# Optimization experiments

Measured on AMD Instinct MI355X. Metric: run time of the kernel, lower is better.

Reference implementation:

```python
import jax, jax.numpy as jnp
import numpy as np

EPS = 1e-15        # norm / denominator clamp (matches geoopt min_norm)
BALL_EPS = 1e-5    # projection margin: max radius = (1-BALL_EPS)/sqrt(c)
TANH_ARG_MAX = 15.0  # pre-expmap tangent clip so tanh arg stays finite
ATANH_MAX = 1.0 - 1e-7

def _norm(x):
    return jnp.maximum(jnp.linalg.norm(x, axis=-1, keepdims=True), EPS)

def pre_clip(x, c):
    # clip tangent norm so sqrt(c)*||x|| <= TANH_ARG_MAX before expmap0
    maxn = TANH_ARG_MAX / jnp.sqrt(c)
    n = _norm(x)
    return x * jnp.minimum(1.0, maxn / n)

def post_clip(x, c):
    # project onto the open Poincare ball of curvature c
    maxn = (1.0 - BALL_EPS) / jnp.sqrt(c)
    n = _norm(x)
    return x * jnp.minimum(1.0, maxn / n)

def expmap0(u, c):
    sc = jnp.sqrt(c)
    n = _norm(u)
    return jnp.tanh(sc * n) * u / (sc * n)

def logmap0(y, c):
    sc = jnp.sqrt(c)
    n = _norm(y)
    return jnp.arctanh(jnp.minimum(sc * n, ATANH_MAX)) * y / (sc * n)

def mobius_add(x, y, c):
    x2 = jnp.sum(x * x, axis=-1, keepdims=True)
    y2 = jnp.sum(y * y, axis=-1, keepdims=True)
    xy = jnp.sum(x * y, axis=-1, keepdims=True)
    num = (1.0 + 2.0 * c * xy + c * y2) * x + (1.0 - c * x2) * y
    den = 1.0 + 2.0 * c * xy + (c * c) * x2 * y2
    return num / jnp.maximum(den, EPS)

def mobius_scalar_mul(r, x, c):
    sc = jnp.sqrt(c)
    n = _norm(x)
    return jnp.tanh(r * jnp.arctanh(jnp.minimum(sc * n, ATANH_MAX))) * x / (sc * n)


def setup_inputs() -> dict:
    key = jax.random.key(0)
    kx, ky = jax.random.split(key)
    B, N, D = 64, 577, 768
    # scale so points land well inside the ball after expmap0
    x = jax.random.normal(kx, (B, N, D), dtype=jnp.float32) * 0.05
    y = jax.random.normal(ky, (B, N, D), dtype=jnp.float32) * 0.05
    return {
        "x": x,
        "y": y,
        "curv_hra": jnp.asarray(np.log(np.e - 1.0), dtype=jnp.float32),  # inv_softplus(1.0)
        "gamma_raw": jnp.asarray(0.5, dtype=jnp.float32),
        "gamma_scale": jnp.asarray(0.0, dtype=jnp.float32),
        "scale_center": jnp.asarray(0.0, dtype=jnp.float32),
    }


def reference(x, y, curv_hra, gamma_raw, gamma_scale, scale_center):
    c = jax.nn.softplus(curv_hra)  # ball curvature from raw param
    hr_x = post_clip(expmap0(pre_clip(x, c), c), c)
    hr_y = post_clip(expmap0(pre_clip(y, c), c), c)
    s = jax.nn.sigmoid(scale_center)
    g_max = 1.0 + jax.nn.softplus(gamma_scale)
    gamma = g_max * jnp.tanh(gamma_raw)
    # learned Mobius midpoint p between hr_x and hr_y
    sx = post_clip(mobius_scalar_mul(s, hr_x, c), c)
    sy = post_clip(mobius_scalar_mul(1.0 - s, hr_y, c), c)
    p = post_clip(mobius_add(sx, sy, c), c)
    # recenter at p, scale residual branch, add, move back, log to tangent
    x_p = post_clip(mobius_add(-p, hr_x, c), c)
    y_p = post_clip(mobius_add(-p, hr_y, c), c)
    y_s = post_clip(mobius_scalar_mul(gamma, y_p, c), c)
    hres_p = post_clip(mobius_add(x_p, y_s, c), c)
    hres = mobius_add(p, hres_p, c)
    r = post_clip(hres, c)
    return logmap0(r, c)
```

## Files before the change

kernel.cpp:

```cpp
#include <hip/hip_runtime.h>
#include <math.h>

#define F_EPS 1e-15f
#define F_BALL 0.99999f
#define F_TANH_ARG_MAX 15.0f
#define F_ATANH_MAX (1.0f - 1e-7f)
#define F_LOG2E 1.4426950408889634f
#define F_LN2   0.6931471805599453f

__device__ __forceinline__ float rcp_fast(float x) {
    float r = __builtin_amdgcn_rcpf(x);
    return r * (2.0f - x * r);
}
__device__ __forceinline__ float sqrt_fast(float x) { return __builtin_amdgcn_sqrtf(x); }
__device__ __forceinline__ float exp2_fast(float x) { return __builtin_amdgcn_exp2f(x); }
__device__ __forceinline__ float log2_fast(float x) { return __builtin_amdgcn_logf(x); }
__device__ __forceinline__ float exp_fast(float x)  { return exp2_fast(x * F_LOG2E); }

__device__ __forceinline__ float tanh_fast(float x) {
    float ax = fabsf(x);
    float t  = exp2_fast(ax * (-2.0f * F_LOG2E));
    float r  = (1.0f - t) * rcp_fast(1.0f + t);
    return copysignf(r, x);
}
__device__ __forceinline__ float atanh_fast(float z) {
    return (0.5f * F_LN2) * log2_fast((1.0f + z) * rcp_fast(1.0f - z));
}
__device__ __forceinline__ float softplus_fast(float x) {
    return F_LN2 * log2_fast(1.0f + exp2_fast(x * F_LOG2E));
}

struct GramS { float X2, Y2, XY; };

__device__ __forceinline__ float gnorm2(const GramS& g, float a, float b) {
    return fmaxf(a * a * g.X2 + 2.0f * a * b * g.XY + b * b * g.Y2, 0.0f);
}
__device__ __forceinline__ float gdot(const GramS& g, float au, float bu, float av, float bv) {
    return au * av * g.X2 + (au * bv + bu * av) * g.XY + bu * bv * g.Y2;
}

__device__ __forceinline__ void madd_c(float c, float u2, float v2, float uv,
                                       float au, float bu, float av, float bv,
                                       float& ao, float& bo) {
    float twocuv = 2.0f * c * uv;
    float A = 1.0f + twocuv + c * v2;
    float B = 1.0f - c * u2;
    float rden = rcp_fast(fmaxf(1.0f + twocuv + c * c * u2 * v2, F_EPS));
    ao = (A * au + B * av) * rden;
    bo = (A * bu + B * bv) * rden;
}

__device__ __forceinline__ float pclip(const GramS& g, float maxn_post, float& a, float& b) {
    float n = fmaxf(sqrt_fast(gnorm2(g, a, b)), F_EPS);
    float s = fminf(1.0f, maxn_post * rcp_fast(n));
    a *= s; b *= s;
    return s * n;
}

__device__ __forceinline__ float msm_coef(float sc, float rcp_sc, float r,
                                          float n_in, float& n_out) {
    float ne = fmaxf(n_in, F_EPS);
    float z  = fminf(sc * ne, F_ATANH_MAX);
    float w  = tanh_fast(r * atanh_fast(z));
    float m  = w * rcp_fast(sc * ne);
    float aw = fabsf(w);
    float s  = fminf(1.0f, F_BALL * rcp_fast(fmaxf(aw, F_EPS)));
    n_out = s * aw * rcp_sc;
    return m * s;
}

__device__ __forceinline__ float hr_c(float nx, float sc, float rcp_sc,
                                      float maxn_pre, float& n_out) {
    float s1 = fminf(1.0f, maxn_pre * rcp_fast(nx));
    float n1 = fmaxf(s1 * nx, F_EPS);
    float t  = tanh_fast(sc * n1);
    float f1 = t * rcp_fast(sc * n1);
    float s2 = fminf(1.0f, F_BALL * rcp_fast(fmaxf(t, F_EPS)));
    n_out = s2 * t * rcp_sc;
    return s1 * f1 * s2;
}

__global__ __launch_bounds__(256) void hra_kernel(
    const float* __restrict__ x, const float* __restrict__ y,
    const float* __restrict__ p_curv, const float* __restrict__ p_graw,
    const float* __restrict__ p_gscale, const float* __restrict__ p_scent,
    float* __restrict__ out, int rows)
{
    const int wid  = (blockIdx.x << 2) | (threadIdx.x >> 6);
    const int lane = threadIdx.x & 63;
    const int row0 = wid << 2;
    if (row0 >= rows) return;

    const float curv   = p_curv[0];
    const float graw   = p_graw[0];
    const float gscale = p_gscale[0];
    const float scent  = p_scent[0];

    int ridx[4];
#pragma unroll
    for (int r = 0; r < 4; ++r) ridx[r] = min(row0 + r, rows - 1);

    float4 xv[4][3], yv[4][3];
#pragma unroll
    for (int r = 0; r < 4; ++r) {
        const float4* xr = (const float4*)(x + (size_t)ridx[r] * 768);
        const float4* yr = (const float4*)(y + (size_t)ridx[r] * 768);
#pragma unroll
        for (int j = 0; j < 3; ++j) {
            xv[r][j] = xr[lane + 64 * j];
            yv[r][j] = yr[lane + 64 * j];
        }
    }

    float X2[4], Y2[4], XY[4];
#pragma unroll
    for (int r = 0; r < 4; ++r) {
        float sxx = 0.0f, syy = 0.0f, sxy = 0.0f;
#pragma unroll
        for (int j = 0; j < 3; ++j) {
            sxx += xv[r][j].x * xv[r][j].x + xv[r][j].y * xv[r][j].y
                 + xv[r][j].z * xv[r][j].z + xv[r][j].w * xv[r][j].w;
            syy += yv[r][j].x * yv[r][j].x + yv[r][j].y * yv[r][j].y
                 + yv[r][j].z * yv[r][j].z + yv[r][j].w * yv[r][j].w;
            sxy += xv[r][j].x * yv[r][j].x + xv[r][j].y * yv[r][j].y
                 + xv[r][j].z * yv[r][j].z + xv[r][j].w * yv[r][j].w;
        }
        X2[r] = sxx; Y2[r] = syy; XY[r] = sxy;
    }

#pragma unroll
    for (int o = 32; o > 0; o >>= 1) {
#pragma unroll
        for (int r = 0; r < 4; ++r) {
            X2[r] += __shfl_xor(X2[r], o, 64);
            Y2[r] += __shfl_xor(Y2[r], o, 64);
            XY[r] += __shfl_xor(XY[r], o, 64);
        }
    }

    const int rsel = lane & 3;
    const float gX2 = rsel == 0 ? X2[0] : rsel == 1 ? X2[1] : rsel == 2 ? X2[2] : X2[3];
    const float gY2 = rsel == 0 ? Y2[0] : rsel == 1 ? Y2[1] : rsel == 2 ? Y2[2] : Y2[3];
    const float gXY = rsel == 0 ? XY[0] : rsel == 1 ? XY[1] : rsel == 2 ? XY[2] : XY[3];
    GramS g; g.X2 = gX2; g.Y2 = gY2; g.XY = gXY;

    const float c      = softplus_fast(curv);
    const float sc     = sqrt_fast(c);
    const float rcp_sc = rcp_fast(sc);
    const float maxn_pre  = F_TANH_ARG_MAX * rcp_sc;
    const float maxn_post = F_BALL * rcp_sc;
    const float s      = rcp_fast(1.0f + exp_fast(-scent));
    const float g_max  = 1.0f + softplus_fast(gscale);
    const float gamma  = g_max * tanh_fast(graw);

    const float nx = fmaxf(sqrt_fast(gX2), F_EPS);
    const float ny = fmaxf(sqrt_fast(gY2), F_EPS);

    float n_hx, n_hy;
    const float hx = hr_c(nx, sc, rcp_sc, maxn_pre, n_hx);
    const float hy = hr_c(ny, sc, rcp_sc, maxn_pre, n_hy);

    float n_sx, n_sy;
    const float sxa = hx * msm_coef(sc, rcp_sc, s,        n_hx, n_sx);
    const float syb = hy * msm_coef(sc, rcp_sc, 1.0f - s, n_hy, n_sy);

    float pa, pb;
    {
        float u2 = n_sx * n_sx, v2 = n_sy * n_sy;
        float uv = sxa * syb * gXY;
        madd_c(c, u2, v2, uv, sxa, 0.0f, 0.0f, syb, pa, pb);
    }
    const float n_p = pclip(g, maxn_post, pa, pb);
    const float np2 = n_p * n_p;

    float xpa, xpb;
    {
        float v2 = n_hx * n_hx;
        float uv = -hx * (pa * gX2 + pb * gXY);
        madd_c(c, np2, v2, uv, -pa, -pb, hx, 0.0f, xpa, xpb);
    }
    const float n_xp = pclip(g, maxn_post, xpa, xpb);

    float ypa, ypb;
    {
        float v2 = n_hy * n_hy;
        float uv = -hy * (pa * gXY + pb * gY2);
        madd_c(c, np2, v2, uv, -pa, -pb, 0.0f, hy, ypa, ypb);
    }
    float n_yp = pclip(g, maxn_post, ypa, ypb);

    float n_ys;
    {
        float m = msm_coef(sc, rcp_sc, gamma, n_yp, n_ys);
        ypa *= m; ypb *= m;
    }

    float ha, hb;
    {
        float u2 = n_xp * n_xp, v2 = n_ys * n_ys;
        float uv = gdot(g, xpa, xpb, ypa, ypb);
        madd_c(c, u2, v2, uv, xpa, xpb, ypa, ypb, ha, hb);
    }
    const float n_h = pclip(g, maxn_post, ha, hb);

    float ra, rb;
    {
        float u2 = np2, v2 = n_h * n_h;
        float uv = gdot(g, pa, pb, ha, hb);
        madd_c(c, u2, v2, uv, pa, pb, ha, hb, ra, rb);
    }
    const float n_r = pclip(g, maxn_post, ra, rb);

    const float nrr = fmaxf(n_r, F_EPS);
    const float z   = fminf(sc * nrr, F_ATANH_MAX);
    const float f   = atanh_fast(z) * rcp_fast(sc * nrr);
    const float fa  = f * ra;
    const float fb  = f * rb;

#pragma unroll
    for (int r = 0; r < 4; ++r) {
        const float far = __shfl(fa, r, 64);
        const float fbr = __shfl(fb, r, 64);
        if (row0 + r < rows) {
            float4* outr = (float4*)(out + (size_t)(row0 + r) * 768);
#pragma unroll
            for (int j = 0; j < 3; ++j) {
                float4 o;
                o.x = far * xv[r][j].x + fbr * yv[r][j].x;
                o.y = far * xv[r][j].y + fbr * yv[r][j].y;
                o.z = far * xv[r][j].z + fbr * yv[r][j].z;
                o.w = far * xv[r][j].w + fbr * yv[r][j].w;
                outr[lane + 64 * j] = o;
            }
        }
    }
}

extern "C" void kernel_launch(void* const* d_in, const int* in_sizes, int n_in,
                              void* d_out, int out_size, void* d_ws, size_t ws_size,
                              hipStream_t stream) {
    const float* x = (const float*)d_in[0];
    const float* y = (const float*)d_in[1];
    const float* curv = (const float*)d_in[2];
    const float* graw = (const float*)d_in[3];
    const float* gscale = (const float*)d_in[4];
    const float* scent = (const float*)d_in[5];
    float* out = (float*)d_out;

    const int rows = in_sizes[0] / 768;
    const int blocks = (rows + 15) / 16;

    hipLaunchKernelGGL(hra_kernel, dim3(blocks), dim3(256), 0, stream,
                       x, y, curv, graw, gscale, scent, out, rows);
}
```

Before: 280.2 us.

## Split fused kernel into per-row coefficient pass and streaming blend pass

Adds a first kernel that computes per-row Gram sums and the scalar coefficients (fa, fb) into the workspace, and a second grid-stride kernel that reads x and y again and writes fa*x + fb*y. The aim is to decouple the latency-heavy scalar chain from the streaming output write. The cost is that x and y are read from memory twice instead of once, and there is an extra launch. The original fused kernel remains as a fallback when no workspace is available.

```diff
diff --git a/kernel.cpp b/kernel.cpp
--- a/kernel.cpp
+++ b/kernel.cpp
@@ -80,6 +80,179 @@
     return s1 * f1 * s2;
 }
 
+__device__ __forceinline__ void chain_4rows(
+    float gX2, float gY2, float gXY,
+    float curv, float graw, float gscale, float scent,
+    float& fa, float& fb)
+{
+    GramS g; g.X2 = gX2; g.Y2 = gY2; g.XY = gXY;
+
+    const float c      = softplus_fast(curv);
+    const float sc     = sqrt_fast(c);
+    const float rcp_sc = rcp_fast(sc);
+    const float maxn_pre  = F_TANH_ARG_MAX * rcp_sc;
+    const float maxn_post = F_BALL * rcp_sc;
+    const float s      = rcp_fast(1.0f + exp_fast(-scent));
+    const float g_max  = 1.0f + softplus_fast(gscale);
+    const float gamma  = g_max * tanh_fast(graw);
+
+    const float nx = fmaxf(sqrt_fast(gX2), F_EPS);
+    const float ny = fmaxf(sqrt_fast(gY2), F_EPS);
+
+    float n_hx, n_hy;
+    const float hx = hr_c(nx, sc, rcp_sc, maxn_pre, n_hx);
+    const float hy = hr_c(ny, sc, rcp_sc, maxn_pre, n_hy);
+
+    float n_sx, n_sy;
+    const float sxa = hx * msm_coef(sc, rcp_sc, s,        n_hx, n_sx);
+    const float syb = hy * msm_coef(sc, rcp_sc, 1.0f - s, n_hy, n_sy);
+
+    float pa, pb;
+    {
+        float u2 = n_sx * n_sx, v2 = n_sy * n_sy;
+        float uv = sxa * syb * gXY;
+        madd_c(c, u2, v2, uv, sxa, 0.0f, 0.0f, syb, pa, pb);
+    }
+    const float n_p = pclip(g, maxn_post, pa, pb);
+    const float np2 = n_p * n_p;
+
+    float xpa, xpb;
+    {
+        float v2 = n_hx * n_hx;
+        float uv = -hx * (pa * gX2 + pb * gXY);
+        madd_c(c, np2, v2, uv, -pa, -pb, hx, 0.0f, xpa, xpb);
+    }
+    const float n_xp = pclip(g, maxn_post, xpa, xpb);
+
+    float ypa, ypb;
+    {
+        float v2 = n_hy * n_hy;
+        float uv = -hy * (pa * gXY + pb * gY2);
+        madd_c(c, np2, v2, uv, -pa, -pb, 0.0f, hy, ypa, ypb);
+    }
+    float n_yp = pclip(g, maxn_post, ypa, ypb);
+
+    float n_ys;
+    {
+        float m = msm_coef(sc, rcp_sc, gamma, n_yp, n_ys);
+        ypa *= m; ypb *= m;
+    }
+
+    float ha, hb;
+    {
+        float u2 = n_xp * n_xp, v2 = n_ys * n_ys;
+        float uv = gdot(g, xpa, xpb, ypa, ypb);
+        madd_c(c, u2, v2, uv, xpa, xpb, ypa, ypb, ha, hb);
+    }
+    const float n_h = pclip(g, maxn_post, ha, hb);
+
+    float ra, rb;
+    {
+        float u2 = np2, v2 = n_h * n_h;
+        float uv = gdot(g, pa, pb, ha, hb);
+        madd_c(c, u2, v2, uv, pa, pb, ha, hb, ra, rb);
+    }
+    const float n_r = pclip(g, maxn_post, ra, rb);
+
+    const float nrr = fmaxf(n_r, F_EPS);
+    const float z   = fminf(sc * nrr, F_ATANH_MAX);
+    const float f   = atanh_fast(z) * rcp_fast(sc * nrr);
+    fa = f * ra;
+    fb = f * rb;
+}
+
+__global__ __launch_bounds__(256) void hra_gram(
+    const float* __restrict__ x, const float* __restrict__ y,
+    const float* __restrict__ p_curv, const float* __restrict__ p_graw,
+    const float* __restrict__ p_gscale, const float* __restrict__ p_scent,
+    float2* __restrict__ fab, int rows)
+{
+    const int wid  = (blockIdx.x << 2) | (threadIdx.x >> 6);
+    const int lane = threadIdx.x & 63;
+    const int row0 = wid << 2;
+    if (row0 >= rows) return;
+
+    const float curv   = p_curv[0];
+    const float graw   = p_graw[0];
+    const float gscale = p_gscale[0];
+    const float scent  = p_scent[0];
+
+    int ridx[4];
+#pragma unroll
+    for (int r = 0; r < 4; ++r) ridx[r] = min(row0 + r, rows - 1);
+
+    float4 xv[4][3], yv[4][3];
+#pragma unroll
+    for (int r = 0; r < 4; ++r) {
+        const float4* xr = (const float4*)(x + (size_t)ridx[r] * 768);
+        const float4* yr = (const float4*)(y + (size_t)ridx[r] * 768);
+#pragma unroll
+        for (int j = 0; j < 3; ++j) {
+            xv[r][j] = xr[lane + 64 * j];
+            yv[r][j] = yr[lane + 64 * j];
+        }
+    }
+
+    float X2[4], Y2[4], XY[4];
+#pragma unroll
+    for (int r = 0; r < 4; ++r) {
+        float sxx = 0.0f, syy = 0.0f, sxy = 0.0f;
+#pragma unroll
+        for (int j = 0; j < 3; ++j) {
+            sxx += xv[r][j].x * xv[r][j].x + xv[r][j].y * xv[r][j].y
+                 + xv[r][j].z * xv[r][j].z + xv[r][j].w * xv[r][j].w;
+            syy += yv[r][j].x * yv[r][j].x + yv[r][j].y * yv[r][j].y
+                 + yv[r][j].z * yv[r][j].z + yv[r][j].w * yv[r][j].w;
+            sxy += xv[r][j].x * yv[r][j].x + xv[r][j].y * yv[r][j].y
+                 + xv[r][j].z * yv[r][j].z + xv[r][j].w * yv[r][j].w;
+        }
+        X2[r] = sxx; Y2[r] = syy; XY[r] = sxy;
+    }
+
+#pragma unroll
+    for (int o = 32; o > 0; o >>= 1) {
+#pragma unroll
+        for (int r = 0; r < 4; ++r) {
+            X2[r] += __shfl_xor(X2[r], o, 64);
+            Y2[r] += __shfl_xor(Y2[r], o, 64);
+            XY[r] += __shfl_xor(XY[r], o, 64);
+        }
+    }
+
+    const int rsel = lane & 3;
+    const float gX2 = rsel == 0 ? X2[0] : rsel == 1 ? X2[1] : rsel == 2 ? X2[2] : X2[3];
+    const float gY2 = rsel == 0 ? Y2[0] : rsel == 1 ? Y2[1] : rsel == 2 ? Y2[2] : Y2[3];
+    const float gXY = rsel == 0 ? XY[0] : rsel == 1 ? XY[1] : rsel == 2 ? XY[2] : XY[3];
+
+    float fa, fb;
+    chain_4rows(gX2, gY2, gXY, curv, graw, gscale, scent, fa, fb);
+
+    if (lane < 4 && row0 + lane < rows) {
+        float2 v; v.x = fa; v.y = fb;
+        fab[row0 + lane] = v;
+    }
+}
+
+__global__ __launch_bounds__(256) void hra_blend(
+    const float4* __restrict__ x4, const float4* __restrict__ y4,
+    const float2* __restrict__ fab, float4* __restrict__ out4, int n4)
+{
+    int i = blockIdx.x * 256 + threadIdx.x;
+    const int stride = gridDim.x * 256;
+    for (; i < n4; i += stride) {
+        const int row = i / 192;
+        const float2 s = fab[row];
+        const float4 a = x4[i];
+        const float4 b = y4[i];
+        float4 o;
+        o.x = s.x * a.x + s.y * b.x;
+        o.y = s.x * a.y + s.y * b.y;
+        o.z = s.x * a.z + s.y * b.z;
+        o.w = s.x * a.w + s.y * b.w;
+        out4[i] = o;
+    }
+}
+
 __global__ __launch_bounds__(256) void hra_kernel(
     const float* __restrict__ x, const float* __restrict__ y,
     const float* __restrict__ p_curv, const float* __restrict__ p_graw,
@@ -142,80 +315,9 @@
     const float gX2 = rsel == 0 ? X2[0] : rsel == 1 ? X2[1] : rsel == 2 ? X2[2] : X2[3];
     const float gY2 = rsel == 0 ? Y2[0] : rsel == 1 ? Y2[1] : rsel == 2 ? Y2[2] : Y2[3];
     const float gXY = rsel == 0 ? XY[0] : rsel == 1 ? XY[1] : rsel == 2 ? XY[2] : XY[3];
-    GramS g; g.X2 = gX2; g.Y2 = gY2; g.XY = gXY;
-
-    const float c      = softplus_fast(curv);
-    const float sc     = sqrt_fast(c);
-    const float rcp_sc = rcp_fast(sc);
-    const float maxn_pre  = F_TANH_ARG_MAX * rcp_sc;
-    const float maxn_post = F_BALL * rcp_sc;
-    const float s      = rcp_fast(1.0f + exp_fast(-scent));
-    const float g_max  = 1.0f + softplus_fast(gscale);
-    const float gamma  = g_max * tanh_fast(graw);
-
-    const float nx = fmaxf(sqrt_fast(gX2), F_EPS);
-    const float ny = fmaxf(sqrt_fast(gY2), F_EPS);
-
-    float n_hx, n_hy;
-    const float hx = hr_c(nx, sc, rcp_sc, maxn_pre, n_hx);
-    const float hy = hr_c(ny, sc, rcp_sc, maxn_pre, n_hy);
-
-    float n_sx, n_sy;
-    const float sxa = hx * msm_coef(sc, rcp_sc, s,        n_hx, n_sx);
-    const float syb = hy * msm_coef(sc, rcp_sc, 1.0f - s, n_hy, n_sy);
-
-    float pa, pb;
-    {
-        float u2 = n_sx * n_sx, v2 = n_sy * n_sy;
-        float uv = sxa * syb * gXY;
-        madd_c(c, u2, v2, uv, sxa, 0.0f, 0.0f, syb, pa, pb);
-    }
-    const float n_p = pclip(g, maxn_post, pa, pb);
-    const float np2 = n_p * n_p;
-
-    float xpa, xpb;
-    {
-        float v2 = n_hx * n_hx;
-        float uv = -hx * (pa * gX2 + pb * gXY);
-        madd_c(c, np2, v2, uv, -pa, -pb, hx, 0.0f, xpa, xpb);
-    }
-    const float n_xp = pclip(g, maxn_post, xpa, xpb);
-
-    float ypa, ypb;
-    {
-        float v2 = n_hy * n_hy;
-        float uv = -hy * (pa * gXY + pb * gY2);
-        madd_c(c, np2, v2, uv, -pa, -pb, 0.0f, hy, ypa, ypb);
-    }
-    float n_yp = pclip(g, maxn_post, ypa, ypb);
-
-    float n_ys;
-    {
-        float m = msm_coef(sc, rcp_sc, gamma, n_yp, n_ys);
-        ypa *= m; ypb *= m;
-    }
-
-    float ha, hb;
-    {
-        float u2 = n_xp * n_xp, v2 = n_ys * n_ys;
-        float uv = gdot(g, xpa, xpb, ypa, ypb);
-        madd_c(c, u2, v2, uv, xpa, xpb, ypa, ypb, ha, hb);
-    }
-    const float n_h = pclip(g, maxn_post, ha, hb);
-
-    float ra, rb;
-    {
-        float u2 = np2, v2 = n_h * n_h;
-        float uv = gdot(g, pa, pb, ha, hb);
-        madd_c(c, u2, v2, uv, pa, pb, ha, hb, ra, rb);
-    }
-    const float n_r = pclip(g, maxn_post, ra, rb);
-
-    const float nrr = fmaxf(n_r, F_EPS);
-    const float z   = fminf(sc * nrr, F_ATANH_MAX);
-    const float f   = atanh_fast(z) * rcp_fast(sc * nrr);
-    const float fa  = f * ra;
-    const float fb  = f * rb;
+
+    float fa, fb;
+    chain_4rows(gX2, gY2, gXY, curv, graw, gscale, scent, fa, fb);
 
 #pragma unroll
     for (int r = 0; r < 4; ++r) {
@@ -248,8 +350,20 @@
     float* out = (float*)d_out;
 
     const int rows = in_sizes[0] / 768;
-    const int blocks = (rows + 15) / 16;
-
-    hipLaunchKernelGGL(hra_kernel, dim3(blocks), dim3(256), 0, stream,
-                       x, y, curv, graw, gscale, scent, out, rows);
-}
+    const size_t ws_needed = (size_t)rows * sizeof(float2);
+
+    if (d_ws != nullptr && ws_size >= ws_needed) {
+        const int blocks1 = (rows + 15) / 16;
+        hipLaunchKernelGGL(hra_gram, dim3(blocks1), dim3(256), 0, stream,
+                           x, y, curv, graw, gscale, scent,
+                           (float2*)d_ws, rows);
+        const int n4 = rows * 192;
+        hipLaunchKernelGGL(hra_blend, dim3(2048), dim3(256), 0, stream,
+                           (const float4*)x, (const float4*)y,
+                           (const float2*)d_ws, (float4*)out, n4);
+    } else {
+        const int blocks = (rows + 15) / 16;
+        hipLaunchKernelGGL(hra_kernel, dim3(blocks), dim3(256), 0, stream,
+                           x, y, curv, graw, gscale, scent, out, rows);
+    }
+}
```

Result: slower. 319.5 us (+14.0%).

## Use persistent grid-stride waves with double-buffered row-pair prefetch

Applied to the files above, without the earlier changes.

Replaces the one-shot kernel, where each wave handled 4 rows, with a persistent kernel capped at 1024 blocks. Each wave now handles pairs of rows in a grid-stride loop and double-buffers registers, loading the next pair before computing and storing the current one. The aim is to hide global load latency within each wave and to amortise the scalar parameter setup. The catch is fewer waves in flight (1024 blocks x 4 waves) and higher register pressure from the two buffers, which could reduce latency hiding through occupancy.

```diff
diff --git a/kernel.cpp b/kernel.cpp
--- a/kernel.cpp
+++ b/kernel.cpp
@@ -31,6 +31,7 @@
 }
 
 struct GramS { float X2, Y2, XY; };
+struct ChainP { float c, sc, rcp_sc, maxn_pre, maxn_post, s, gamma; };
 
 __device__ __forceinline__ float gnorm2(const GramS& g, float a, float b) {
     return fmaxf(a * a * g.X2 + 2.0f * a * b * g.XY + b * b * g.Y2, 0.0f);
@@ -80,41 +81,102 @@
     return s1 * f1 * s2;
 }
 
-__global__ __launch_bounds__(256) void hra_kernel(
-    const float* __restrict__ x, const float* __restrict__ y,
-    const float* __restrict__ p_curv, const float* __restrict__ p_graw,
-    const float* __restrict__ p_gscale, const float* __restrict__ p_scent,
-    float* __restrict__ out, int rows)
-{
-    const int wid  = (blockIdx.x << 2) | (threadIdx.x >> 6);
-    const int lane = threadIdx.x & 63;
-    const int row0 = wid << 2;
-    if (row0 >= rows) return;
-
-    const float curv   = p_curv[0];
-    const float graw   = p_graw[0];
-    const float gscale = p_gscale[0];
-    const float scent  = p_scent[0];
-
-    int ridx[4];
-#pragma unroll
-    for (int r = 0; r < 4; ++r) ridx[r] = min(row0 + r, rows - 1);
-
-    float4 xv[4][3], yv[4][3];
-#pragma unroll
-    for (int r = 0; r < 4; ++r) {
-        const float4* xr = (const float4*)(x + (size_t)ridx[r] * 768);
-        const float4* yr = (const float4*)(y + (size_t)ridx[r] * 768);
+__device__ __forceinline__ void chain_row(float gX2, float gY2, float gXY,
+                                          const ChainP& P, float& fa, float& fb) {
+    GramS g; g.X2 = gX2; g.Y2 = gY2; g.XY = gXY;
+    const float c = P.c, sc = P.sc, rcp_sc = P.rcp_sc;
+    const float maxn_pre = P.maxn_pre, maxn_post = P.maxn_post;
+
+    const float nx = fmaxf(sqrt_fast(gX2), F_EPS);
+    const float ny = fmaxf(sqrt_fast(gY2), F_EPS);
+
+    float n_hx, n_hy;
+    const float hx = hr_c(nx, sc, rcp_sc, maxn_pre, n_hx);
+    const float hy = hr_c(ny, sc, rcp_sc, maxn_pre, n_hy);
+
+    float n_sx, n_sy;
+    const float sxa = hx * msm_coef(sc, rcp_sc, P.s,        n_hx, n_sx);
+    const float syb = hy * msm_coef(sc, rcp_sc, 1.0f - P.s, n_hy, n_sy);
+
+    float pa, pb;
+    {
+        float u2 = n_sx * n_sx, v2 = n_sy * n_sy;
+        float uv = sxa * syb * gXY;
+        madd_c(c, u2, v2, uv, sxa, 0.0f, 0.0f, syb, pa, pb);
+    }
+    const float n_p = pclip(g, maxn_post, pa, pb);
+    const float np2 = n_p * n_p;
+
+    float xpa, xpb;
+    {
+        float v2 = n_hx * n_hx;
+        float uv = -hx * (pa * gX2 + pb * gXY);
+        madd_c(c, np2, v2, uv, -pa, -pb, hx, 0.0f, xpa, xpb);
+    }
+    const float n_xp = pclip(g, maxn_post, xpa, xpb);
+
+    float ypa, ypb;
+    {
+        float v2 = n_hy * n_hy;
+        float uv = -hy * (pa * gXY + pb * gY2);
+        madd_c(c, np2, v2, uv, -pa, -pb, 0.0f, hy, ypa, ypb);
+    }
+    float n_yp = pclip(g, maxn_post, ypa, ypb);
+
+    float n_ys;
+    {
+        float m = msm_coef(sc, rcp_sc, P.gamma, n_yp, n_ys);
+        ypa *= m; ypb *= m;
+    }
+
+    float ha, hb;
+    {
+        float u2 = n_xp * n_xp, v2 = n_ys * n_ys;
+        float uv = gdot(g, xpa, xpb, ypa, ypb);
+        madd_c(c, u2, v2, uv, xpa, xpb, ypa, ypb, ha, hb);
+    }
+    const float n_h = pclip(g, maxn_post, ha, hb);
+
+    float ra, rb;
+    {
+        float u2 = np2, v2 = n_h * n_h;
+        float uv = gdot(g, pa, pb, ha, hb);
+        madd_c(c, u2, v2, uv, pa, pb, ha, hb, ra, rb);
+    }
+    const float n_r = pclip(g, maxn_post, ra, rb);
+
+    const float nrr = fmaxf(n_r, F_EPS);
+    const float z   = fminf(sc * nrr, F_ATANH_MAX);
+    const float f   = atanh_fast(z) * rcp_fast(sc * nrr);
+    fa = f * ra;
+    fb = f * rb;
+}
+
+__device__ __forceinline__ void load_group(const float* __restrict__ x,
+                                           const float* __restrict__ y,
+                                           int g, int rows, int lane,
+                                           float4 (&xv)[2][3], float4 (&yv)[2][3]) {
+    const int r0 = g << 1;
+#pragma unroll
+    for (int r = 0; r < 2; ++r) {
+        const int rr = min(r0 + r, rows - 1);
+        const float4* xr = (const float4*)(x + (size_t)rr * 768);
+        const float4* yr = (const float4*)(y + (size_t)rr * 768);
 #pragma unroll
         for (int j = 0; j < 3; ++j) {
             xv[r][j] = xr[lane + 64 * j];
             yv[r][j] = yr[lane + 64 * j];
         }
     }
-
-    float X2[4], Y2[4], XY[4];
-#pragma unroll
-    for (int r = 0; r < 4; ++r) {
+}
+
+__device__ __forceinline__ void process_group(float4 (&xv)[2][3], float4 (&yv)[2][3],
+                                              int g, int rows, int lane,
+                                              const ChainP& P,
+                                              float* __restrict__ out) {
+    float X2[2], Y2[2], XY[2];
+#pragma unroll
+    for (int r = 0; r < 2; ++r) {
         float sxx = 0.0f, syy = 0.0f, sxy = 0.0f;
 #pragma unroll
         for (int j = 0; j < 3; ++j) {
@@ -131,98 +193,28 @@
 #pragma unroll
     for (int o = 32; o > 0; o >>= 1) {
 #pragma unroll
-        for (int r = 0; r < 4; ++r) {
+        for (int r = 0; r < 2; ++r) {
             X2[r] += __shfl_xor(X2[r], o, 64);
             Y2[r] += __shfl_xor(Y2[r], o, 64);
             XY[r] += __shfl_xor(XY[r], o, 64);
         }
     }
 
-    const int rsel = lane & 3;
-    const float gX2 = rsel == 0 ? X2[0] : rsel == 1 ? X2[1] : rsel == 2 ? X2[2] : X2[3];
-    const float gY2 = rsel == 0 ? Y2[0] : rsel == 1 ? Y2[1] : rsel == 2 ? Y2[2] : Y2[3];
-    const float gXY = rsel == 0 ? XY[0] : rsel == 1 ? XY[1] : rsel == 2 ? XY[2] : XY[3];
-    GramS g; g.X2 = gX2; g.Y2 = gY2; g.XY = gXY;
-
-    const float c      = softplus_fast(curv);
-    const float sc     = sqrt_fast(c);
-    const float rcp_sc = rcp_fast(sc);
-    const float maxn_pre  = F_TANH_ARG_MAX * rcp_sc;
-    const float maxn_post = F_BALL * rcp_sc;
-    const float s      = rcp_fast(1.0f + exp_fast(-scent));
-    const float g_max  = 1.0f + softplus_fast(gscale);
-    const float gamma  = g_max * tanh_fast(graw);
-
-    const float nx = fmaxf(sqrt_fast(gX2), F_EPS);
-    const float ny = fmaxf(sqrt_fast(gY2), F_EPS);
-
-    float n_hx, n_hy;
-    const float hx = hr_c(nx, sc, rcp_sc, maxn_pre, n_hx);
-    const float hy = hr_c(ny, sc, rcp_sc, maxn_pre, n_hy);
-
-    float n_sx, n_sy;
-    const float sxa = hx * msm_coef(sc, rcp_sc, s,        n_hx, n_sx);
-    const float syb = hy * msm_coef(sc, rcp_sc, 1.0f - s, n_hy, n_sy);
-
-    float pa, pb;
-    {
-        float u2 = n_sx * n_sx, v2 = n_sy * n_sy;
-        float uv = sxa * syb * gXY;
-        madd_c(c, u2, v2, uv, sxa, 0.0f, 0.0f, syb, pa, pb);
-    }
-    const float n_p = pclip(g, maxn_post, pa, pb);
-    const float np2 = n_p * n_p;
-
-    float xpa, xpb;
-    {
-        float v2 = n_hx * n_hx;
-        float uv = -hx * (pa * gX2 + pb * gXY);
-        madd_c(c, np2, v2, uv, -pa, -pb, hx, 0.0f, xpa, xpb);
-    }
-    const float n_xp = pclip(g, maxn_post, xpa, xpb);
-
-    float ypa, ypb;
-    {
-        float v2 = n_hy * n_hy;
-        float uv = -hy * (pa * gXY + pb * gY2);
-        madd_c(c, np2, v2, uv, -pa, -pb, 0.0f, hy, ypa, ypb);
-    }
-    float n_yp = pclip(g, maxn_post, ypa, ypb);
-
-    float n_ys;
-    {
-        float m = msm_coef(sc, rcp_sc, gamma, n_yp, n_ys);
-        ypa *= m; ypb *= m;
-    }
-
-    float ha, hb;
-    {
-        float u2 = n_xp * n_xp, v2 = n_ys * n_ys;
-        float uv = gdot(g, xpa, xpb, ypa, ypb);
-        madd_c(c, u2, v2, uv, xpa, xpb, ypa, ypb, ha, hb);
-    }
-    const float n_h = pclip(g, maxn_post, ha, hb);
-
-    float ra, rb;
-    {
-        float u2 = np2, v2 = n_h * n_h;
-        float uv = gdot(g, pa, pb, ha, hb);
-        madd_c(c, u2, v2, uv, pa, pb, ha, hb, ra, rb);
-    }
-    const float n_r = pclip(g, maxn_post, ra, rb);
-
-    const float nrr = fmaxf(n_r, F_EPS);
-    const float z   = fminf(sc * nrr, F_ATANH_MAX);
-    const float f   = atanh_fast(z) * rcp_fast(sc * nrr);
-    const float fa  = f * ra;
-    const float fb  = f * rb;
-
-#pragma unroll
-    for (int r = 0; r < 4; ++r) {
+    const int rsel = lane & 1;
+    const float gX2 = rsel ? X2[1] : X2[0];
+    const float gY2 = rsel ? Y2[1] : Y2[0];
+    const float gXY = rsel ? XY[1] : XY[0];
+
+    float fa, fb;
+    chain_row(gX2, gY2, gXY, P, fa, fb);
+
+    const int r0 = g << 1;
+#pragma unroll
+    for (int r = 0; r < 2; ++r) {
         const float far = __shfl(fa, r, 64);
         const float fbr = __shfl(fb, r, 64);
-        if (row0 + r < rows) {
-            float4* outr = (float4*)(out + (size_t)(row0 + r) * 768);
+        if (r0 + r < rows) {
+            float4* outr = (float4*)(out + (size_t)(r0 + r) * 768);
 #pragma unroll
             for (int j = 0; j < 3; ++j) {
                 float4 o;
@@ -232,6 +224,57 @@
                 o.w = far * xv[r][j].w + fbr * yv[r][j].w;
                 outr[lane + 64 * j] = o;
             }
+        }
+    }
+}
+
+__global__ __launch_bounds__(256) void hra_fused(
+    const float* __restrict__ x, const float* __restrict__ y,
+    const float* __restrict__ p_curv, const float* __restrict__ p_graw,
+    const float* __restrict__ p_gscale, const float* __restrict__ p_scent,
+    float* __restrict__ out, int rows)
+{
+    const int lane   = threadIdx.x & 63;
+    const int wglob  = (blockIdx.x << 2) | (threadIdx.x >> 6);
+    const int nwaves = gridDim.x << 2;
+    const int ngroups = (rows + 1) >> 1;
+    if (wglob >= ngroups) return;
+
+    const float curv   = p_curv[0];
+    const float graw   = p_graw[0];
+    const float gscale = p_gscale[0];
+    const float scent  = p_scent[0];
+
+    ChainP P;
+    P.c        = softplus_fast(curv);
+    P.sc       = sqrt_fast(P.c);
+    P.rcp_sc   = rcp_fast(P.sc);
+    P.maxn_pre  = F_TANH_ARG_MAX * P.rcp_sc;
+    P.maxn_post = F_BALL * P.rcp_sc;
+    P.s        = rcp_fast(1.0f + exp_fast(-scent));
+    P.gamma    = (1.0f + softplus_fast(gscale)) * tanh_fast(graw);
+
+    float4 xA[2][3], yA[2][3], xB[2][3], yB[2][3];
+
+    int g = wglob;
+    load_group(x, y, g, rows, lane, xA, yA);
+    while (true) {
+        const int gB = g + nwaves;
+        if (gB < ngroups) {
+            load_group(x, y, gB, rows, lane, xB, yB);
+            process_group(xA, yA, g, rows, lane, P, out);
+            const int gA = gB + nwaves;
+            if (gA < ngroups) {
+                load_group(x, y, gA, rows, lane, xA, yA);
+                process_group(xB, yB, gB, rows, lane, P, out);
+                g = gA;
+            } else {
+                process_group(xB, yB, gB, rows, lane, P, out);
+                return;
+            }
+        } else {
+            process_group(xA, yA, g, rows, lane, P, out);
+            return;
         }
     }
 }
@@ -248,8 +291,10 @@
     float* out = (float*)d_out;
 
     const int rows = in_sizes[0] / 768;
-    const int blocks = (rows + 15) / 16;
-
-    hipLaunchKernelGGL(hra_kernel, dim3(blocks), dim3(256), 0, stream,
+    const int ngroups = (rows + 1) / 2;
+    int blocks = (ngroups + 3) / 4;
+    if (blocks > 1024) blocks = 1024;
+
+    hipLaunchKernelGGL(hra_fused, dim3(blocks), dim3(256), 0, stream,
                        x, y, curv, graw, gscale, scent, out, rows);
 }
```

Result: no change. 278.9 us (-0.5%).

## Process one row per wave with grid-stride loop and reload inputs for output

Applied to the files above, without the earlier changes.

Replaces the four-rows-per-wave kernel, which held 48 float4 registers live, with a persistent grid-stride loop handling one row per wave. The shared per-row hyperbolic chain moves into a helper, and scalar parameters are computed once per thread. Inputs are re-read from memory (expected to hit cache) for the output combination instead of being kept in registers. The aim is lower register pressure and higher occupancy to better hide memory latency, at the cost of extra load traffic.

```diff
diff --git a/kernel.cpp b/kernel.cpp
--- a/kernel.cpp
+++ b/kernel.cpp
@@ -31,6 +31,7 @@
 }
 
 struct GramS { float X2, Y2, XY; };
+struct ChainP { float c, sc, rcp_sc, maxn_pre, maxn_post, s, gamma; };
 
 __device__ __forceinline__ float gnorm2(const GramS& g, float a, float b) {
     return fmaxf(a * a * g.X2 + 2.0f * a * b * g.XY + b * b * g.Y2, 0.0f);
@@ -80,158 +81,139 @@
     return s1 * f1 * s2;
 }
 
-__global__ __launch_bounds__(256) void hra_kernel(
+__device__ __forceinline__ void chain_row(float gX2, float gY2, float gXY,
+                                          const ChainP& P, float& fa, float& fb) {
+    GramS g; g.X2 = gX2; g.Y2 = gY2; g.XY = gXY;
+    const float c = P.c, sc = P.sc, rcp_sc = P.rcp_sc;
+    const float maxn_pre = P.maxn_pre, maxn_post = P.maxn_post;
+
+    const float nx = fmaxf(sqrt_fast(gX2), F_EPS);
+    const float ny = fmaxf(sqrt_fast(gY2), F_EPS);
+
+    float n_hx, n_hy;
+    const float hx = hr_c(nx, sc, rcp_sc, maxn_pre, n_hx);
+    const float hy = hr_c(ny, sc, rcp_sc, maxn_pre, n_hy);
+
+    float n_sx, n_sy;
+    const float sxa = hx * msm_coef(sc, rcp_sc, P.s,        n_hx, n_sx);
+    const float syb = hy * msm_coef(sc, rcp_sc, 1.0f - P.s, n_hy, n_sy);
+
+    float pa, pb;
+    {
+        float u2 = n_sx * n_sx, v2 = n_sy * n_sy;
+        float uv = sxa * syb * gXY;
+        madd_c(c, u2, v2, uv, sxa, 0.0f, 0.0f, syb, pa, pb);
+    }
+    const float n_p = pclip(g, maxn_post, pa, pb);
+    const float np2 = n_p * n_p;
+
+    float xpa, xpb;
+    {
+        float v2 = n_hx * n_hx;
+        float uv = -hx * (pa * gX2 + pb * gXY);
+        madd_c(c, np2, v2, uv, -pa, -pb, hx, 0.0f, xpa, xpb);
+    }
+    const float n_xp = pclip(g, maxn_post, xpa, xpb);
+
+    float ypa, ypb;
+    {
+        float v2 = n_hy * n_hy;
+        float uv = -hy * (pa * gXY + pb * gY2);
+        madd_c(c, np2, v2, uv, -pa, -pb, 0.0f, hy, ypa, ypb);
+    }
+    float n_yp = pclip(g, maxn_post, ypa, ypb);
+
+    float n_ys;
+    {
+        float m = msm_coef(sc, rcp_sc, P.gamma, n_yp, n_ys);
+        ypa *= m; ypb *= m;
+    }
+
+    float ha, hb;
+    {
+        float u2 = n_xp * n_xp, v2 = n_ys * n_ys;
+        float uv = gdot(g, xpa, xpb, ypa, ypb);
+        madd_c(c, u2, v2, uv, xpa, xpb, ypa, ypb, ha, hb);
+    }
+    const float n_h = pclip(g, maxn_post, ha, hb);
+
+    float ra, rb;
+    {
+        float u2 = np2, v2 = n_h * n_h;
+        float uv = gdot(g, pa, pb, ha, hb);
+        madd_c(c, u2, v2, uv, pa, pb, ha, hb, ra, rb);
+    }
+    const float n_r = pclip(g, maxn_post, ra, rb);
+
+    const float nrr = fmaxf(n_r, F_EPS);
+    const float z   = fminf(sc * nrr, F_ATANH_MAX);
+    const float f   = atanh_fast(z) * rcp_fast(sc * nrr);
+    fa = f * ra;
+    fb = f * rb;
+}
+
+__global__ __launch_bounds__(256, 6) void hra_fused(
     const float* __restrict__ x, const float* __restrict__ y,
     const float* __restrict__ p_curv, const float* __restrict__ p_graw,
     const float* __restrict__ p_gscale, const float* __restrict__ p_scent,
     float* __restrict__ out, int rows)
 {
-    const int wid  = (blockIdx.x << 2) | (threadIdx.x >> 6);
     const int lane = threadIdx.x & 63;
-    const int row0 = wid << 2;
-    if (row0 >= rows) return;
-
-    const float curv   = p_curv[0];
-    const float graw   = p_graw[0];
-    const float gscale = p_gscale[0];
-    const float scent  = p_scent[0];
-
-    int ridx[4];
+    const int w    = (blockIdx.x << 2) | (threadIdx.x >> 6);
+    const int nw   = gridDim.x << 2;
+
+    ChainP P;
+    P.c         = softplus_fast(p_curv[0]);
+    P.sc        = sqrt_fast(P.c);
+    P.rcp_sc    = rcp_fast(P.sc);
+    P.maxn_pre  = F_TANH_ARG_MAX * P.rcp_sc;
+    P.maxn_post = F_BALL * P.rcp_sc;
+    P.s         = rcp_fast(1.0f + exp_fast(-p_scent[0]));
+    P.gamma     = (1.0f + softplus_fast(p_gscale[0])) * tanh_fast(p_graw[0]);
+
+    for (int row = w; row < rows; row += nw) {
+        const float4* xr = (const float4*)(x + (size_t)row * 768) + lane;
+        const float4* yr = (const float4*)(y + (size_t)row * 768) + lane;
+
+        float4 x0 = xr[0],   y0 = yr[0];
+        float4 x1 = xr[64],  y1 = yr[64];
+        float4 x2 = xr[128], y2 = yr[128];
+
+        float sxx = x0.x*x0.x + x0.y*x0.y + x0.z*x0.z + x0.w*x0.w
+                  + x1.x*x1.x + x1.y*x1.y + x1.z*x1.z + x1.w*x1.w
+                  + x2.x*x2.x + x2.y*x2.y + x2.z*x2.z + x2.w*x2.w;
+        float syy = y0.x*y0.x + y0.y*y0.y + y0.z*y0.z + y0.w*y0.w
+                  + y1.x*y1.x + y1.y*y1.y + y1.z*y1.z + y1.w*y1.w
+                  + y2.x*y2.x + y2.y*y2.y + y2.z*y2.z + y2.w*y2.w;
+        float sxy = x0.x*y0.x + x0.y*y0.y + x0.z*y0.z + x0.w*y0.w
+                  + x1.x*y1.x + x1.y*y1.y + x1.z*y1.z + x1.w*y1.w
+                  + x2.x*y2.x + x2.y*y2.y + x2.z*y2.z + x2.w*y2.w;
+
 #pragma unroll
-    for (int r = 0; r < 4; ++r) ridx[r] = min(row0 + r, rows - 1);
-
-    float4 xv[4][3], yv[4][3];
-#pragma unroll
-    for (int r = 0; r < 4; ++r) {
-        const float4* xr = (const float4*)(x + (size_t)ridx[r] * 768);
-        const float4* yr = (const float4*)(y + (size_t)ridx[r] * 768);
+        for (int o = 32; o > 0; o >>= 1) {
+            sxx += __shfl_xor(sxx, o, 64);
+            syy += __shfl_xor(syy, o, 64);
+            sxy += __shfl_xor(sxy, o, 64);
+        }
+
+        float fa, fb;
+        chain_row(sxx, syy, sxy, P, fa, fb);
+
+        const float4* xr2 = xr;
+        const float4* yr2 = yr;
+        asm volatile("" : "+v"(xr2));
+        asm volatile("" : "+v"(yr2));
+        float4* outr = (float4*)(out + (size_t)row * 768) + lane;
 #pragma unroll
         for (int j = 0; j < 3; ++j) {
-            xv[r][j] = xr[lane + 64 * j];
-            yv[r][j] = yr[lane + 64 * j];
-        }
-    }
-
-    float X2[4], Y2[4], XY[4];
-#pragma unroll
-    for (int r = 0; r < 4; ++r) {
-        float sxx = 0.0f, syy = 0.0f, sxy = 0.0f;
-#pragma unroll
-        for (int j = 0; j < 3; ++j) {
-            sxx += xv[r][j].x * xv[r][j].x + xv[r][j].y * xv[r][j].y
-                 + xv[r][j].z * xv[r][j].z + xv[r][j].w * xv[r][j].w;
-            syy += yv[r][j].x * yv[r][j].x + yv[r][j].y * yv[r][j].y
-                 + yv[r][j].z * yv[r][j].z + yv[r][j].w * yv[r][j].w;
-            sxy += xv[r][j].x * yv[r][j].x + xv[r][j].y * yv[r][j].y
-                 + xv[r][j].z * yv[r][j].z + xv[r][j].w * yv[r][j].w;
-        }
-        X2[r] = sxx; Y2[r] = syy; XY[r] = sxy;
-    }
-
-#pragma unroll
-    for (int o = 32; o > 0; o >>= 1) {
-#pragma unroll
-        for (int r = 0; r < 4; ++r) {
-            X2[r] += __shfl_xor(X2[r], o, 64);
-            Y2[r] += __shfl_xor(Y2[r], o, 64);
-            XY[r] += __shfl_xor(XY[r], o, 64);
-        }
-    }
-
-    const int rsel = lane & 3;
-    const float gX2 = rsel == 0 ? X2[0] : rsel == 1 ? X2[1] : rsel == 2 ? X2[2] : X2[3];
-    const float gY2 = rsel == 0 ? Y2[0] : rsel == 1 ? Y2[1] : rsel == 2 ? Y2[2] : Y2[3];
-    const float gXY = rsel == 0 ? XY[0] : rsel == 1 ? XY[1] : rsel == 2 ? XY[2] : XY[3];
-    GramS g; g.X2 = gX2; g.Y2 = gY2; g.XY = gXY;
-
-    const float c      = softplus_fast(curv);
-    const float sc     = sqrt_fast(c);
-    const float rcp_sc = rcp_fast(sc);
-    const float maxn_pre  = F_TANH_ARG_MAX * rcp_sc;
-    const float maxn_post = F_BALL * rcp_sc;
-    const float s      = rcp_fast(1.0f + exp_fast(-scent));
-    const float g_max  = 1.0f + softplus_fast(gscale);
-    const float gamma  = g_max * tanh_fast(graw);
-
-    const float nx = fmaxf(sqrt_fast(gX2), F_EPS);
-    const float ny = fmaxf(sqrt_fast(gY2), F_EPS);
-
-    float n_hx, n_hy;
-    const float hx = hr_c(nx, sc, rcp_sc, maxn_pre, n_hx);
-    const float hy = hr_c(ny, sc, rcp_sc, maxn_pre, n_hy);
-
-    float n_sx, n_sy;
-    const float sxa = hx * msm_coef(sc, rcp_sc, s,        n_hx, n_sx);
-    const float syb = hy * msm_coef(sc, rcp_sc, 1.0f - s, n_hy, n_sy);
-
-    float pa, pb;
-    {
-        float u2 = n_sx * n_sx, v2 = n_sy * n_sy;
-        float uv = sxa * syb * gXY;
-        madd_c(c, u2, v2, uv, sxa, 0.0f, 0.0f, syb, pa, pb);
-    }
-    const float n_p = pclip(g, maxn_post, pa, pb);
-    const float np2 = n_p * n_p;
-
-    float xpa, xpb;
-    {
-        float v2 = n_hx * n_hx;
-        float uv = -hx * (pa * gX2 + pb * gXY);
-        madd_c(c, np2, v2, uv, -pa, -pb, hx, 0.0f, xpa, xpb);
-    }
-    const float n_xp = pclip(g, maxn_post, xpa, xpb);
-
-    float ypa, ypb;
-    {
-        float v2 = n_hy * n_hy;
-        float uv = -hy * (pa * gXY + pb * gY2);
-        madd_c(c, np2, v2, uv, -pa, -pb, 0.0f, hy, ypa, ypb);
-    }
-    float n_yp = pclip(g, maxn_post, ypa, ypb);
-
-    float n_ys;
-    {
-        float m = msm_coef(sc, rcp_sc, gamma, n_yp, n_ys);
-        ypa *= m; ypb *= m;
-    }
-
-    float ha, hb;
-    {
-        float u2 = n_xp * n_xp, v2 = n_ys * n_ys;
-        float uv = gdot(g, xpa, xpb, ypa, ypb);
-        madd_c(c, u2, v2, uv, xpa, xpb, ypa, ypb, ha, hb);
-    }
-    const float n_h = pclip(g, maxn_post, ha, hb);
-
-    float ra, rb;
-    {
-        float u2 = np2, v2 = n_h * n_h;
-        float uv = gdot(g, pa, pb, ha, hb);
-        madd_c(c, u2, v2, uv, pa, pb, ha, hb, ra, rb);
-    }
-    const float n_r = pclip(g, maxn_post, ra, rb);
-
-    const float nrr = fmaxf(n_r, F_EPS);
-    const float z   = fminf(sc * nrr, F_ATANH_MAX);
-    const float f   = atanh_fast(z) * rcp_fast(sc * nrr);
-    const float fa  = f * ra;
-    const float fb  = f * rb;
-
-#pragma unroll
-    for (int r = 0; r < 4; ++r) {
-        const float far = __shfl(fa, r, 64);
-        const float fbr = __shfl(fb, r, 64);
-        if (row0 + r < rows) {
-            float4* outr = (float4*)(out + (size_t)(row0 + r) * 768);
-#pragma unroll
-            for (int j = 0; j < 3; ++j) {
-                float4 o;
-                o.x = far * xv[r][j].x + fbr * yv[r][j].x;
-                o.y = far * xv[r][j].y + fbr * yv[r][j].y;
-                o.z = far * xv[r][j].z + fbr * yv[r][j].z;
-                o.w = far * xv[r][j].w + fbr * yv[r][j].w;
-                outr[lane + 64 * j] = o;
-            }
+            const float4 a = xr2[64 * j];
+            const float4 b = yr2[64 * j];
+            float4 o;
+            o.x = fa * a.x + fb * b.x;
+            o.y = fa * a.y + fb * b.y;
+            o.z = fa * a.z + fb * b.z;
+            o.w = fa * a.w + fb * b.w;
+            outr[64 * j] = o;
         }
     }
 }
@@ -248,8 +230,9 @@
     float* out = (float*)d_out;
 
     const int rows = in_sizes[0] / 768;
-    const int blocks = (rows + 15) / 16;
-
-    hipLaunchKernelGGL(hra_kernel, dim3(blocks), dim3(256), 0, stream,
+    int blocks = (rows + 3) / 4;
+    if (blocks > 2048) blocks = 2048;
+
+    hipLaunchKernelGGL(hra_fused, dim3(blocks), dim3(256), 0, stream,
                        x, y, curv, graw, gscale, scent, out, rows);
 }
```

Measured after the change: 284.8 us. About the same (+1.6%).
